# Optimization experiments

Hardware: AMD Instinct MI355X
Metric: run time of the kernel (lower is better)

The kernel has to match this reference:

```python
import jax, jax.numpy as jnp
import numpy as np

B, D_IN, D_ATT, N_PROTO = 262144, 512, 32, 4
GAMMA = 2.0
SCALE = D_ATT ** -0.5
LN_EPS = 1e-5


def setup_inputs() -> dict:
    key = jax.random.key(0)
    ks = jax.random.split(key, 8)
    return {
        "x": jax.random.normal(ks[0], (B, D_IN), dtype=jnp.float32),
        "minority_prob": jax.random.uniform(ks[1], (B,), dtype=jnp.float32),
        "Wq": jax.random.normal(ks[2], (D_ATT, D_IN), dtype=jnp.float32) * (D_IN ** -0.5),
        "bq": jnp.zeros((D_ATT,), dtype=jnp.float32),
        "proto_keys": jax.random.normal(ks[3], (N_PROTO, D_ATT), dtype=jnp.float32) * 0.02,
        "proto_values": jax.random.normal(ks[4], (N_PROTO, D_ATT), dtype=jnp.float32) * 0.02,
        "proto_importance": jnp.ones((N_PROTO,), dtype=jnp.float32) / N_PROTO,
        "focal_alpha": jnp.array([0.6], dtype=jnp.float32),
        "focal_temp": jnp.array([1.0], dtype=jnp.float32),
        "Wo": jax.random.normal(ks[5], (D_ATT, D_ATT), dtype=jnp.float32) * (D_ATT ** -0.5),
        "bo": jnp.zeros((D_ATT,), dtype=jnp.float32),
        "ln_gamma": jnp.ones((D_ATT,), dtype=jnp.float32),
        "ln_beta": jnp.zeros((D_ATT,), dtype=jnp.float32),
    }


def reference(x, minority_prob, Wq, bq, proto_keys, proto_values,
              proto_importance, focal_alpha, focal_temp, Wo, bo, ln_gamma, ln_beta):
    # query projection: [B, D_ATT]
    q = x @ Wq.T + bq
    # prototype scores: [B, N_PROTO]
    scores = q @ proto_keys.T + proto_importance[None, :]
    # focal modulation (per-sample weight broadcast over prototypes)
    uncertainty = 1.0 - jnp.abs(minority_prob - 0.5) * 2.0
    focal_w = focal_alpha * jnp.power(uncertainty + 1e-8, GAMMA) * focal_temp
    scores = scores * (1.0 + focal_w[:, None])
    # softmax over prototypes (dropout is identity at inference)
    weights = jax.nn.softmax(scores * SCALE, axis=-1)
    # attend prototype values: [B, D_ATT]
    attended = weights @ proto_values
    out = attended @ Wo.T + bo
    # layer norm
    mu = jnp.mean(out, axis=-1, keepdims=True)
    var = jnp.var(out, axis=-1, keepdims=True)
    out = (out - mu) * jax.lax.rsqrt(var + LN_EPS) * ln_gamma + ln_beta
    return out, weights
```

## Files before the change

### kernel.cpp

```cpp
#include <hip/hip_runtime.h>

#define B_TOTAL 262144
#define D_IN 512
#define LN_EPS 1e-5f

typedef __attribute__((ext_vector_type(8))) short short8;
typedef __attribute__((ext_vector_type(4))) float f32x4;

__device__ __forceinline__ unsigned short f2bf_rne(float f) {
    union { float f; unsigned int u; } c; c.f = f;
    unsigned int u = c.u;
    u += 0x7fffu + ((u >> 16) & 1u);
    return (unsigned short)(u >> 16);
}

__device__ __forceinline__ short8 cvt8(f32x4 lo, f32x4 hi) {
    short8 r;
    r[0] = (short)f2bf_rne(lo[0]); r[1] = (short)f2bf_rne(lo[1]);
    r[2] = (short)f2bf_rne(lo[2]); r[3] = (short)f2bf_rne(lo[3]);
    r[4] = (short)f2bf_rne(hi[0]); r[5] = (short)f2bf_rne(hi[1]);
    r[6] = (short)f2bf_rne(hi[2]); r[7] = (short)f2bf_rne(hi[3]);
    return r;
}

__global__ __launch_bounds__(256) void faiia_kernel(
    const float* __restrict__ x,
    const float* __restrict__ mprob,
    const float* __restrict__ Wq,
    const float* __restrict__ bq,
    const float* __restrict__ pk,
    const float* __restrict__ pv,
    const float* __restrict__ imp,
    const float* __restrict__ falpha,
    const float* __restrict__ ftemp,
    const float* __restrict__ Wo,
    const float* __restrict__ bo,
    const float* __restrict__ gamma,
    const float* __restrict__ beta,
    float* __restrict__ out)
{
    __shared__ float lds_q[64][33];
    __shared__ float lds_att[64][33];

    const int tid  = threadIdx.x;
    const int wave = tid >> 6;
    const int lane = tid & 63;
    const int blockBase = blockIdx.x * 64;

    const int m    = lane & 15;
    const int quad = lane >> 4;
    const int row  = blockBase + wave * 16 + m;

    const float* ax  = x  + (size_t)row * D_IN + quad * 8;
    const float* bw0 = Wq + (size_t)m   * D_IN + quad * 8;
    const float* bw1 = bw0 + 16 * D_IN;

    f32x4 acc0 = {0.f, 0.f, 0.f, 0.f};
    f32x4 acc1 = {0.f, 0.f, 0.f, 0.f};
    #pragma unroll
    for (int kk = 0; kk < 16; ++kk) {
        f32x4 a0 = *(const f32x4*)(ax  + kk * 32);
        f32x4 a1 = *(const f32x4*)(ax  + kk * 32 + 4);
        f32x4 p0 = *(const f32x4*)(bw0 + kk * 32);
        f32x4 p1 = *(const f32x4*)(bw0 + kk * 32 + 4);
        f32x4 r0 = *(const f32x4*)(bw1 + kk * 32);
        f32x4 r1 = *(const f32x4*)(bw1 + kk * 32 + 4);
        short8 a  = cvt8(a0, a1);
        short8 b0 = cvt8(p0, p1);
        short8 b1 = cvt8(r0, r1);
        acc0 = __builtin_amdgcn_mfma_f32_16x16x32_bf16(a, b0, acc0, 0, 0, 0);
        acc1 = __builtin_amdgcn_mfma_f32_16x16x32_bf16(a, b1, acc1, 0, 0, 0);
    }

    {
        const float bq0 = bq[m];
        const float bq1 = bq[m + 16];
        #pragma unroll
        for (int r = 0; r < 4; ++r) {
            int s = wave * 16 + quad * 4 + r;
            lds_q[s][m]      = acc0[r] + bq0;
            lds_q[s][m + 16] = acc1[r] + bq1;
        }
    }
    __syncthreads();

    const int sLocal = tid >> 2;
    const int part   = tid & 3;
    const int d0     = part * 8;
    const int sample = blockBase + sLocal;

    float q8[8];
    #pragma unroll
    for (int j = 0; j < 8; ++j) q8[j] = lds_q[sLocal][d0 + j];

    float sc[4];
    #pragma unroll
    for (int p = 0; p < 4; ++p) {
        float s = 0.f;
        #pragma unroll
        for (int j = 0; j < 8; ++j) s += q8[j] * pk[p * 32 + d0 + j];
        s += __shfl_xor(s, 1);
        s += __shfl_xor(s, 2);
        sc[p] = s + imp[p];
    }

    const float prob = mprob[sample];
    const float unc  = 1.f - fabsf(prob - 0.5f) * 2.f;
    const float ue   = unc + 1e-8f;
    const float fw   = falpha[0] * ue * ue * ftemp[0];
    const float SCALE = 0.1767766952966369f;
    const float mult  = (1.f + fw) * SCALE;

    float z[4];
    #pragma unroll
    for (int p = 0; p < 4; ++p) z[p] = sc[p] * mult;
    float zmax = fmaxf(fmaxf(z[0], z[1]), fmaxf(z[2], z[3]));
    float w[4], wsum = 0.f;
    #pragma unroll
    for (int p = 0; p < 4; ++p) { w[p] = expf(z[p] - zmax); wsum += w[p]; }
    const float winv = 1.f / wsum;
    #pragma unroll
    for (int p = 0; p < 4; ++p) w[p] *= winv;

    #pragma unroll
    for (int j = 0; j < 8; ++j) {
        float a = 0.f;
        #pragma unroll
        for (int p = 0; p < 4; ++p) a += w[p] * pv[p * 32 + d0 + j];
        lds_att[sLocal][d0 + j] = a;
    }
    __syncthreads();

    float att[32];
    #pragma unroll
    for (int n = 0; n < 32; ++n) att[n] = lds_att[sLocal][n];

    float o[8];
    #pragma unroll
    for (int jo = 0; jo < 8; ++jo) {
        const int n2 = d0 + jo;
        float s = bo[n2];
        #pragma unroll
        for (int n = 0; n < 32; ++n) s += att[n] * Wo[n2 * 32 + n];
        o[jo] = s;
    }

    float s1 = 0.f, s2 = 0.f;
    #pragma unroll
    for (int jo = 0; jo < 8; ++jo) { s1 += o[jo]; s2 += o[jo] * o[jo]; }
    s1 += __shfl_xor(s1, 1); s1 += __shfl_xor(s1, 2);
    s2 += __shfl_xor(s2, 1); s2 += __shfl_xor(s2, 2);
    const float mu   = s1 * (1.f / 32.f);
    const float var  = s2 * (1.f / 32.f) - mu * mu;
    const float rstd = rsqrtf(var + LN_EPS);

    f32x4 res_lo, res_hi;
    #pragma unroll
    for (int jo = 0; jo < 8; ++jo) {
        const int n2 = d0 + jo;
        float y = (o[jo] - mu) * rstd * gamma[n2] + beta[n2];
        if (jo < 4) res_lo[jo] = y; else res_hi[jo - 4] = y;
    }
    *(f32x4*)(out + (size_t)sample * 32 + d0)     = res_lo;
    *(f32x4*)(out + (size_t)sample * 32 + d0 + 4) = res_hi;

    if (part == 0) {
        f32x4 wres;
        #pragma unroll
        for (int p = 0; p < 4; ++p) wres[p] = w[p];
        *(f32x4*)(out + (size_t)B_TOTAL * 32 + (size_t)sample * 4) = wres;
    }
}

extern "C" void kernel_launch(void* const* d_in, const int* in_sizes, int n_in,
                              void* d_out, int out_size, void* d_ws, size_t ws_size,
                              hipStream_t stream) {
    const float* x      = (const float*)d_in[0];
    const float* mprob  = (const float*)d_in[1];
    const float* Wq     = (const float*)d_in[2];
    const float* bq     = (const float*)d_in[3];
    const float* pk     = (const float*)d_in[4];
    const float* pv     = (const float*)d_in[5];
    const float* imp    = (const float*)d_in[6];
    const float* falpha = (const float*)d_in[7];
    const float* ftemp  = (const float*)d_in[8];
    const float* Wo     = (const float*)d_in[9];
    const float* bo     = (const float*)d_in[10];
    const float* gamma  = (const float*)d_in[11];
    const float* beta   = (const float*)d_in[12];
    float* out = (float*)d_out;

    const int blocks = B_TOTAL / 64;
    faiia_kernel<<<blocks, 256, 0, stream>>>(
        x, mprob, Wq, bq, pk, pv, imp, falpha, ftemp, Wo, bo, gamma, beta, out);
}
```

Baseline: 858.2 us.

## Use hardware bf16 conversion, nontemporal x/out accesses, and vectorized LDS traffic

Replaces the manual round-to-nearest-even bf16 conversion with the compiler's __bf16 cast, which may lower to native conversion instructions. Marks the streaming loads of x and the output stores as nontemporal to reduce cache pollution. Pads the LDS tiles to 36 floats with 16-byte alignment so per-thread reads and writes can use 128-bit LDS accesses, and vectorizes the Wo and prototype weight reads. The kernel reads about 512 MB of x, so it is memory-bound and the compute-side changes may not matter much. The wider padding may also change LDS bank-conflict behavior.

```diff
diff --git a/kernel.cpp b/kernel.cpp
--- a/kernel.cpp
+++ b/kernel.cpp
@@ -7,19 +7,19 @@
 typedef __attribute__((ext_vector_type(8))) short short8;
 typedef __attribute__((ext_vector_type(4))) float f32x4;
 
-__device__ __forceinline__ unsigned short f2bf_rne(float f) {
-    union { float f; unsigned int u; } c; c.f = f;
-    unsigned int u = c.u;
-    u += 0x7fffu + ((u >> 16) & 1u);
-    return (unsigned short)(u >> 16);
+__device__ __forceinline__ short f2bf(float f) {
+    __bf16 h = (__bf16)f;
+    unsigned short u;
+    __builtin_memcpy(&u, &h, sizeof(u));
+    return (short)u;
 }
 
 __device__ __forceinline__ short8 cvt8(f32x4 lo, f32x4 hi) {
     short8 r;
-    r[0] = (short)f2bf_rne(lo[0]); r[1] = (short)f2bf_rne(lo[1]);
-    r[2] = (short)f2bf_rne(lo[2]); r[3] = (short)f2bf_rne(lo[3]);
-    r[4] = (short)f2bf_rne(hi[0]); r[5] = (short)f2bf_rne(hi[1]);
-    r[6] = (short)f2bf_rne(hi[2]); r[7] = (short)f2bf_rne(hi[3]);
+    r[0] = f2bf(lo[0]); r[1] = f2bf(lo[1]);
+    r[2] = f2bf(lo[2]); r[3] = f2bf(lo[3]);
+    r[4] = f2bf(hi[0]); r[5] = f2bf(hi[1]);
+    r[6] = f2bf(hi[2]); r[7] = f2bf(hi[3]);
     return r;
 }
 
@@ -39,8 +39,8 @@
     const float* __restrict__ beta,
     float* __restrict__ out)
 {
-    __shared__ float lds_q[64][33];
-    __shared__ float lds_att[64][33];
+    __shared__ __align__(16) float lds_q[64][36];
+    __shared__ __align__(16) float lds_att[64][36];
 
     const int tid  = threadIdx.x;
     const int wave = tid >> 6;
@@ -59,8 +59,8 @@
     f32x4 acc1 = {0.f, 0.f, 0.f, 0.f};
     #pragma unroll
     for (int kk = 0; kk < 16; ++kk) {
-        f32x4 a0 = *(const f32x4*)(ax  + kk * 32);
-        f32x4 a1 = *(const f32x4*)(ax  + kk * 32 + 4);
+        f32x4 a0 = __builtin_nontemporal_load((const f32x4*)(ax + kk * 32));
+        f32x4 a1 = __builtin_nontemporal_load((const f32x4*)(ax + kk * 32 + 4));
         f32x4 p0 = *(const f32x4*)(bw0 + kk * 32);
         f32x4 p1 = *(const f32x4*)(bw0 + kk * 32 + 4);
         f32x4 r0 = *(const f32x4*)(bw1 + kk * 32);
@@ -89,16 +89,16 @@
     const int d0     = part * 8;
     const int sample = blockBase + sLocal;
 
-    float q8[8];
-    #pragma unroll
-    for (int j = 0; j < 8; ++j) q8[j] = lds_q[sLocal][d0 + j];
+    const f32x4 q0v = *(const f32x4*)&lds_q[sLocal][d0];
+    const f32x4 q1v = *(const f32x4*)&lds_q[sLocal][d0 + 4];
 
     float sc[4];
     #pragma unroll
     for (int p = 0; p < 4; ++p) {
-        float s = 0.f;
-        #pragma unroll
-        for (int j = 0; j < 8; ++j) s += q8[j] * pk[p * 32 + d0 + j];
+        const f32x4 k0 = *(const f32x4*)(pk + p * 32 + d0);
+        const f32x4 k1 = *(const f32x4*)(pk + p * 32 + d0 + 4);
+        float s = q0v[0]*k0[0] + q0v[1]*k0[1] + q0v[2]*k0[2] + q0v[3]*k0[3]
+                + q1v[0]*k1[0] + q1v[1]*k1[1] + q1v[2]*k1[2] + q1v[3]*k1[3];
         s += __shfl_xor(s, 1);
         s += __shfl_xor(s, 2);
         sc[p] = s + imp[p];
@@ -122,26 +122,38 @@
     #pragma unroll
     for (int p = 0; p < 4; ++p) w[p] *= winv;
 
-    #pragma unroll
-    for (int j = 0; j < 8; ++j) {
-        float a = 0.f;
-        #pragma unroll
-        for (int p = 0; p < 4; ++p) a += w[p] * pv[p * 32 + d0 + j];
-        lds_att[sLocal][d0 + j] = a;
-    }
+    f32x4 alo, ahi;
+    #pragma unroll
+    for (int j = 0; j < 4; ++j) {
+        const int n = d0 + j;
+        alo[j] = w[0]*pv[n] + w[1]*pv[32 + n] + w[2]*pv[64 + n] + w[3]*pv[96 + n];
+    }
+    #pragma unroll
+    for (int j = 0; j < 4; ++j) {
+        const int n = d0 + 4 + j;
+        ahi[j] = w[0]*pv[n] + w[1]*pv[32 + n] + w[2]*pv[64 + n] + w[3]*pv[96 + n];
+    }
+    *(f32x4*)&lds_att[sLocal][d0]     = alo;
+    *(f32x4*)&lds_att[sLocal][d0 + 4] = ahi;
     __syncthreads();
 
-    float att[32];
-    #pragma unroll
-    for (int n = 0; n < 32; ++n) att[n] = lds_att[sLocal][n];
+    f32x4 attv[8];
+    #pragma unroll
+    for (int c = 0; c < 8; ++c)
+        attv[c] = *(const f32x4*)&lds_att[sLocal][c * 4];
 
     float o[8];
     #pragma unroll
     for (int jo = 0; jo < 8; ++jo) {
         const int n2 = d0 + jo;
+        const f32x4* wrow = (const f32x4*)(Wo + n2 * 32);
         float s = bo[n2];
         #pragma unroll
-        for (int n = 0; n < 32; ++n) s += att[n] * Wo[n2 * 32 + n];
+        for (int c = 0; c < 8; ++c) {
+            f32x4 wv = wrow[c];
+            s += attv[c][0]*wv[0] + attv[c][1]*wv[1]
+               + attv[c][2]*wv[2] + attv[c][3]*wv[3];
+        }
         o[jo] = s;
     }
 
@@ -161,14 +173,15 @@
         float y = (o[jo] - mu) * rstd * gamma[n2] + beta[n2];
         if (jo < 4) res_lo[jo] = y; else res_hi[jo - 4] = y;
     }
-    *(f32x4*)(out + (size_t)sample * 32 + d0)     = res_lo;
-    *(f32x4*)(out + (size_t)sample * 32 + d0 + 4) = res_hi;
+    __builtin_nontemporal_store(res_lo, (f32x4*)(out + (size_t)sample * 32 + d0));
+    __builtin_nontemporal_store(res_hi, (f32x4*)(out + (size_t)sample * 32 + d0 + 4));
 
     if (part == 0) {
         f32x4 wres;
         #pragma unroll
         for (int p = 0; p < 4; ++p) wres[p] = w[p];
-        *(f32x4*)(out + (size_t)B_TOTAL * 32 + (size_t)sample * 4) = wres;
+        __builtin_nontemporal_store(wres,
+            (f32x4*)(out + (size_t)B_TOTAL * 32 + (size_t)sample * 4));
     }
 }
 
```

Result: slower. 878.5 us (+2.4%).
